# Kernel optimization log

Hardware: AMD Instinct MI355X
Metric: run time of the kernel (lower is better)

## Reference

```python
import jax, jax.numpy as jnp
import numpy as np

N_NODES = 20000
N_EDGES = 320000


def _gcn_conv(x, src, dst, dinv, W, b, n):
    # PyG GCNConv: h = x W; out[dst] += deg_src^-1/2 * deg_dst^-1/2 * h[src]; out += b
    h = x @ W                                  # [N, H]
    norm = dinv[src] * dinv[dst]               # [E+N]
    msg = h[src] * norm[:, None]               # [E+N, H]
    out = jax.ops.segment_sum(msg, dst, num_segments=n)
    return out + b


def setup_inputs() -> dict:
    key = jax.random.key(0)
    ks = jax.random.split(key, 11)
    d, c = 256, 3
    sc = 1.0 / np.sqrt(d)
    return {
        "x": jax.random.normal(ks[0], (N_NODES, d), dtype=jnp.float32),
        "edge_index": jax.random.randint(ks[1], (2, N_EDGES), 0, N_NODES, dtype=jnp.int64),
        "W_embed": jax.random.normal(ks[2], (d, d), dtype=jnp.float32) * sc,
        "b_embed": jax.random.normal(ks[3], (d,), dtype=jnp.float32) * 0.01,
        "W1": jax.random.normal(ks[4], (d, d), dtype=jnp.float32) * sc,
        "b1": jax.random.normal(ks[5], (d,), dtype=jnp.float32) * 0.01,
        "W2": jax.random.normal(ks[6], (d, d), dtype=jnp.float32) * sc,
        "b2": jax.random.normal(ks[7], (d,), dtype=jnp.float32) * 0.01,
        "W_cls": jax.random.normal(ks[8], (d, c), dtype=jnp.float32) * sc,
        "b_cls": jax.random.normal(ks[9], (c,), dtype=jnp.float32) * 0.01,
    }


def reference(x, edge_index, W_embed, b_embed, W1, b1, W2, b2, W_cls, b_cls):
    n = x.shape[0]
    # add self-loops once (GCNConv default add_self_loops=True)
    loops = jnp.arange(n, dtype=edge_index.dtype)
    src = jnp.concatenate([edge_index[0], loops])
    dst = jnp.concatenate([edge_index[1], loops])
    # symmetric normalization: degree computed on destination nodes
    deg = jnp.zeros((n,), dtype=x.dtype).at[dst].add(1.0)
    dinv = jax.lax.rsqrt(deg)  # deg >= 1 due to self loops

    h = jax.nn.relu(x @ W_embed + b_embed)
    h = _gcn_conv(h, src, dst, dinv, W1, b1, n)
    h = _gcn_conv(h, src, dst, dinv, W2, b2, n)
    logits = h @ W_cls + b_cls
    return logits
```

## Files before the change

kernel.cpp:

```cpp
#include <hip/hip_runtime.h>
#include <stdint.h>


typedef __attribute__((ext_vector_type(8))) __bf16 bf16x8;
typedef __attribute__((ext_vector_type(4))) float f32x4;

static __device__ __forceinline__ unsigned short f32_to_bf16(float f) {
  uint32_t u = __float_as_uint(f);
  u += 0x7fffu + ((u >> 16) & 1u);
  return (unsigned short)(u >> 16);
}
static __device__ __forceinline__ float bf16_to_f32(unsigned short h) {
  return __uint_as_float(((uint32_t)h) << 16);
}
static __device__ __forceinline__ int frag_addr(int m, int k) {
  return (((m >> 4) * 8 + (k >> 5)) << 9) + (((m & 15) + 16 * ((k >> 3) & 3)) << 3) + (k & 7);
}

__global__ void zero_ints(int* __restrict__ p, int n) {
  int i = blockIdx.x * blockDim.x + threadIdx.x;
  if (i < n) p[i] = 0;
}

__global__ void detect_i64(const unsigned int* __restrict__ ei, int nwords,
                           int* __restrict__ flag) {
  __shared__ int any;
  if (threadIdx.x == 0) any = 0;
  __syncthreads();
  for (int i = 1 + 2 * (int)threadIdx.x; i < nwords; i += 2 * blockDim.x)
    if (ei[i] != 0u) any = 1;
  __syncthreads();
  if (threadIdx.x == 0) *flag = (any == 0) ? 1 : 0;
}

__global__ void count_deg(const int* __restrict__ ei, int E,
                          const int* __restrict__ flag, int* __restrict__ cnt) {
  int e = blockIdx.x * blockDim.x + threadIdx.x;
  int is64 = *flag;
  if (e < E) {
    int d = is64 ? ei[2 * (E + e)] : ei[E + e];
    atomicAdd(&cnt[d], 1);
  }
}

__global__ __launch_bounds__(256) void scan_partials(
    const int* __restrict__ cnt, int* __restrict__ partials, int n) {
  __shared__ int sdata[256];
  int i = blockIdx.x * 256 + threadIdx.x;
  sdata[threadIdx.x] = (i < n) ? cnt[i] : 0;
  __syncthreads();
  for (int off = 128; off > 0; off >>= 1) {
    if (threadIdx.x < off) sdata[threadIdx.x] += sdata[threadIdx.x + off];
    __syncthreads();
  }
  if (threadIdx.x == 0) partials[blockIdx.x] = sdata[0];
}

__global__ __launch_bounds__(1024) void scan_offsets(int* __restrict__ partials,
                                                     int nb) {
  __shared__ int sdata[1024];
  int tid = threadIdx.x;
  sdata[tid] = (tid < nb) ? partials[tid] : 0;
  __syncthreads();
  for (int off = 1; off < 1024; off <<= 1) {
    int t = (tid >= off) ? sdata[tid - off] : 0;
    __syncthreads();
    sdata[tid] += t;
    __syncthreads();
  }
  if (tid < nb) partials[tid] = sdata[tid];
}

__global__ __launch_bounds__(256) void scan_finalize(
    const int* __restrict__ cnt, const int* __restrict__ partials_inc,
    int* __restrict__ row_ptr, float* __restrict__ dinv, int n) {
  __shared__ int sdata[256];
  int b = blockIdx.x;
  int i = b * 256 + threadIdx.x;
  int v = (i < n) ? cnt[i] : 0;
  sdata[threadIdx.x] = v;
  __syncthreads();
  for (int off = 1; off < 256; off <<= 1) {
    int t = (threadIdx.x >= off) ? sdata[threadIdx.x - off] : 0;
    __syncthreads();
    sdata[threadIdx.x] += t;
    __syncthreads();
  }
  int incl = sdata[threadIdx.x];
  int base = (b > 0) ? partials_inc[b - 1] : 0;
  if (i < n) {
    row_ptr[i] = base + incl - v;
    dinv[i] = 1.0f / sqrtf((float)(v + 1));
    if (i == n - 1) row_ptr[n] = base + incl;
  }
}

__global__ void fill_csr(const int* __restrict__ ei, int E,
                         const int* __restrict__ flag,
                         const int* __restrict__ row_ptr, int* __restrict__ cursor,
                         int* __restrict__ csr_src) {
  int e = blockIdx.x * blockDim.x + threadIdx.x;
  int is64 = *flag;
  if (e < E) {
    int s = is64 ? ei[2 * e] : ei[e];
    int d = is64 ? ei[2 * (E + e)] : ei[E + e];
    int pos = row_ptr[d] + atomicAdd(&cursor[d], 1);
    csr_src[pos] = s;
  }
}

__global__ void split_x_frag(const float4* __restrict__ in,
                             unsigned short* __restrict__ hi,
                             unsigned short* __restrict__ lo, int M) {
  int t = blockIdx.x * blockDim.x + threadIdx.x;
  if (t >= M * 32) return;
  int m = t >> 5, o = t & 31;
  float4 v0 = in[m * 64 + o * 2];
  float4 v1 = in[m * 64 + o * 2 + 1];
  float f[8] = {v0.x, v0.y, v0.z, v0.w, v1.x, v1.y, v1.z, v1.w};
  unsigned short hs[8], ls[8];
#pragma unroll
  for (int j = 0; j < 8; ++j) {
    unsigned short h = f32_to_bf16(f[j]);
    hs[j] = h;
    ls[j] = f32_to_bf16(f[j] - bf16_to_f32(h));
  }
  int addr = frag_addr(m, o * 8);
  *(ushort4*)(hi + addr) = make_ushort4(hs[0], hs[1], hs[2], hs[3]);
  *(ushort4*)(hi + addr + 4) = make_ushort4(hs[4], hs[5], hs[6], hs[7]);
  *(ushort4*)(lo + addr) = make_ushort4(ls[0], ls[1], ls[2], ls[3]);
  *(ushort4*)(lo + addr + 4) = make_ushort4(ls[4], ls[5], ls[6], ls[7]);
}

__global__ void pack_w_frag(const float* __restrict__ W,
                            unsigned short* __restrict__ hi,
                            unsigned short* __restrict__ lo) {
  int k = blockIdx.x, n = threadIdx.x;
  float v = W[k * 256 + n];
  unsigned short h = f32_to_bf16(v);
  int addr = frag_addr(n, k);
  hi[addr] = h;
  lo[addr] = f32_to_bf16(v - bf16_to_f32(h));
}

__global__ __launch_bounds__(256) void tail_matvec3(
    const float* __restrict__ A, const float* __restrict__ B3,
    float* __restrict__ O3) {
  int wid = threadIdx.x >> 6, lane = threadIdx.x & 63;
  int k = blockIdx.x * 4 + wid;
  float4 a = ((const float4*)(A + k * 256))[lane];
  int n0 = lane * 4;
  float s0 = a.x * B3[n0 * 3 + 0] + a.y * B3[n0 * 3 + 3] +
             a.z * B3[n0 * 3 + 6] + a.w * B3[n0 * 3 + 9];
  float s1 = a.x * B3[n0 * 3 + 1] + a.y * B3[n0 * 3 + 4] +
             a.z * B3[n0 * 3 + 7] + a.w * B3[n0 * 3 + 10];
  float s2 = a.x * B3[n0 * 3 + 2] + a.y * B3[n0 * 3 + 5] +
             a.z * B3[n0 * 3 + 8] + a.w * B3[n0 * 3 + 11];
#pragma unroll
  for (int off = 32; off > 0; off >>= 1) {
    s0 += __shfl_down(s0, off);
    s1 += __shfl_down(s1, off);
    s2 += __shfl_down(s2, off);
  }
  if (lane == 0) {
    O3[k * 3 + 0] = s0;
    O3[k * 3 + 1] = s1;
    O3[k * 3 + 2] = s2;
  }
}

__global__ __launch_bounds__(128) void tail_vec(
    const float* __restrict__ b1, const float* __restrict__ w2wc,
    const float* __restrict__ b2, const float* __restrict__ Wc,
    const float* __restrict__ bc, float* __restrict__ q,
    float* __restrict__ bvec) {
  int wid = threadIdx.x >> 6, lane = threadIdx.x & 63;
  const float* vin = (wid == 0) ? b1 : b2;
  const float* mat = (wid == 0) ? w2wc : Wc;
  float4 a = ((const float4*)vin)[lane];
  int n0 = lane * 4;
  float s0 = a.x * mat[n0 * 3 + 0] + a.y * mat[n0 * 3 + 3] +
             a.z * mat[n0 * 3 + 6] + a.w * mat[n0 * 3 + 9];
  float s1 = a.x * mat[n0 * 3 + 1] + a.y * mat[n0 * 3 + 4] +
             a.z * mat[n0 * 3 + 7] + a.w * mat[n0 * 3 + 10];
  float s2 = a.x * mat[n0 * 3 + 2] + a.y * mat[n0 * 3 + 5] +
             a.z * mat[n0 * 3 + 8] + a.w * mat[n0 * 3 + 11];
#pragma unroll
  for (int off = 32; off > 0; off >>= 1) {
    s0 += __shfl_down(s0, off);
    s1 += __shfl_down(s1, off);
    s2 += __shfl_down(s2, off);
  }
  if (lane == 0) {
    if (wid == 0) {
      q[0] = s0; q[1] = s1; q[2] = s2;
    } else {
      bvec[0] = s0 + bc[0]; bvec[1] = s1 + bc[1]; bvec[2] = s2 + bc[2];
    }
  }
}

__global__ __launch_bounds__(256) void gemm_u(
    const unsigned short* __restrict__ Ahi, const unsigned short* __restrict__ Alo,
    const unsigned short* __restrict__ Bhi, const unsigned short* __restrict__ Blo,
    int M, const float* __restrict__ bias, const float* __restrict__ P,
    float* __restrict__ u) {
  int wid = threadIdx.x >> 6, lane = threadIdx.x & 63;
  int wm = wid & 1, wn = wid >> 1;
  int Mtiles = (M + 15) >> 4;
  int mt_base = blockIdx.x * 4 + wm * 2;
  int nt_base = blockIdx.y * 8 + wn * 4;
  int la8 = lane * 8;

  int mt0 = mt_base < Mtiles ? mt_base : Mtiles - 1;
  int mt1 = mt_base + 1 < Mtiles ? mt_base + 1 : Mtiles - 1;
  const unsigned short* a0h = Ahi + mt0 * 4096 + la8;
  const unsigned short* a0l = Alo + mt0 * 4096 + la8;
  const unsigned short* a1h = Ahi + mt1 * 4096 + la8;
  const unsigned short* a1l = Alo + mt1 * 4096 + la8;
  const unsigned short* bh = Bhi + nt_base * 4096 + la8;
  const unsigned short* bl = Blo + nt_base * 4096 + la8;

  f32x4 acc[2][4] = {};
#pragma unroll
  for (int k0 = 0; k0 < 8; ++k0) {
    bf16x8 A0h = *(const bf16x8*)(a0h + k0 * 512);
    bf16x8 A0l = *(const bf16x8*)(a0l + k0 * 512);
    bf16x8 A1h = *(const bf16x8*)(a1h + k0 * 512);
    bf16x8 A1l = *(const bf16x8*)(a1l + k0 * 512);
#pragma unroll
    for (int ni = 0; ni < 4; ++ni) {
      bf16x8 Bh = *(const bf16x8*)(bh + ni * 4096 + k0 * 512);
      bf16x8 Bl = *(const bf16x8*)(bl + ni * 4096 + k0 * 512);
      acc[0][ni] = __builtin_amdgcn_mfma_f32_16x16x32_bf16(A0h, Bh, acc[0][ni], 0, 0, 0);
      acc[0][ni] = __builtin_amdgcn_mfma_f32_16x16x32_bf16(A0h, Bl, acc[0][ni], 0, 0, 0);
      acc[0][ni] = __builtin_amdgcn_mfma_f32_16x16x32_bf16(A0l, Bh, acc[0][ni], 0, 0, 0);
      acc[1][ni] = __builtin_amdgcn_mfma_f32_16x16x32_bf16(A1h, Bh, acc[1][ni], 0, 0, 0);
      acc[1][ni] = __builtin_amdgcn_mfma_f32_16x16x32_bf16(A1h, Bl, acc[1][ni], 0, 0, 0);
      acc[1][ni] = __builtin_amdgcn_mfma_f32_16x16x32_bf16(A1l, Bh, acc[1][ni], 0, 0, 0);
    }
  }

  int r = lane & 15, g = lane >> 4;
  float rp[8][3];
#pragma unroll
  for (int t = 0; t < 8; ++t) { rp[t][0] = 0.f; rp[t][1] = 0.f; rp[t][2] = 0.f; }
#pragma unroll
  for (int mi = 0; mi < 2; ++mi) {
#pragma unroll
    for (int ii = 0; ii < 4; ++ii) {
      int ri = mi * 4 + ii;
#pragma unroll
      for (int ni = 0; ni < 4; ++ni) {
        int col = (nt_base + ni) * 16 + r;
        float v = fmaxf(acc[mi][ni][ii] + bias[col], 0.0f);
        rp[ri][0] += v * P[col * 3 + 0];
        rp[ri][1] += v * P[col * 3 + 1];
        rp[ri][2] += v * P[col * 3 + 2];
      }
    }
  }
#pragma unroll
  for (int t = 0; t < 8; ++t) {
#pragma unroll
    for (int c = 0; c < 3; ++c) {
      float v = rp[t][c];
      v += __shfl_down(v, 8, 16);
      v += __shfl_down(v, 4, 16);
      v += __shfl_down(v, 2, 16);
      v += __shfl_down(v, 1, 16);
      rp[t][c] = v;
    }
  }
  if (r == 0) {
#pragma unroll
    for (int mi = 0; mi < 2; ++mi) {
#pragma unroll
      for (int ii = 0; ii < 4; ++ii) {
        int row = (mt_base + mi) * 16 + g * 4 + ii;
        if (row < M) {
          int ri = mi * 4 + ii;
          atomicAdd(&u[row * 3 + 0], rp[ri][0]);
          atomicAdd(&u[row * 3 + 1], rp[ri][1]);
          atomicAdd(&u[row * 3 + 2], rp[ri][2]);
        }
      }
    }
  }
}

__global__ void build_t4a(const float* __restrict__ u, const float* __restrict__ dinv,
                          float4* __restrict__ t4a, int n) {
  int i = blockIdx.x * blockDim.x + threadIdx.x;
  if (i >= n) return;
  float d = dinv[i];
  t4a[i] = make_float4(d * u[i * 3 + 0], d * u[i * 3 + 1], d * u[i * 3 + 2], d);
}

__global__ void conv_skinnyA(const float4* __restrict__ t4a,
                             const int* __restrict__ row_ptr,
                             const int* __restrict__ csr_src,
                             const float* __restrict__ dinv,
                             float4* __restrict__ t4b, int n) {
  int i = blockIdx.x * blockDim.x + threadIdx.x;
  if (i >= n) return;
  int e = row_ptr[i], e1 = row_ptr[i + 1];
  float a0 = 0.f, a1 = 0.f, a2 = 0.f, a3 = 0.f;
  float b0 = 0.f, b1 = 0.f, b2 = 0.f, b3 = 0.f;
  for (; e + 1 < e1; e += 2) {
    float4 v0 = t4a[csr_src[e]];
    float4 v1 = t4a[csr_src[e + 1]];
    a0 += v0.x; a1 += v0.y; a2 += v0.z; a3 += v0.w;
    b0 += v1.x; b1 += v1.y; b2 += v1.z; b3 += v1.w;
  }
  if (e < e1) {
    float4 v0 = t4a[csr_src[e]];
    a0 += v0.x; a1 += v0.y; a2 += v0.z; a3 += v0.w;
  }
  float4 self = t4a[i];
  float d = dinv[i];
  float d2 = d * d;
  t4b[i] = make_float4(d2 * (a0 + b0 + self.x), d2 * (a1 + b1 + self.y),
                       d2 * (a2 + b2 + self.z), d * (a3 + b3 + self.w));
}

__global__ void conv_skinnyB(const float4* __restrict__ t4b,
                             const int* __restrict__ row_ptr,
                             const int* __restrict__ csr_src,
                             const float* __restrict__ dinv,
                             const float* __restrict__ q,
                             const float* __restrict__ bvec,
                             float* __restrict__ out, int n) {
  int i = blockIdx.x * blockDim.x + threadIdx.x;
  if (i >= n) return;
  int e = row_ptr[i], e1 = row_ptr[i + 1];
  float a0 = 0.f, a1 = 0.f, a2 = 0.f;
  float b0 = 0.f, b1 = 0.f, b2 = 0.f;
  for (; e + 1 < e1; e += 2) {
    float4 v0 = t4b[csr_src[e]];
    float4 v1 = t4b[csr_src[e + 1]];
    a0 += v0.x; a1 += v0.y; a2 += v0.z;
    b0 += v1.x; b1 += v1.y; b2 += v1.z;
  }
  if (e < e1) {
    float4 v0 = t4b[csr_src[e]];
    a0 += v0.x; a1 += v0.y; a2 += v0.z;
  }
  float4 self = t4b[i];
  float d = dinv[i];
  float r = self.w;
  out[i * 3 + 0] = d * (a0 + b0 + self.x) + q[0] * r + bvec[0];
  out[i * 3 + 1] = d * (a1 + b1 + self.y) + q[1] * r + bvec[1];
  out[i * 3 + 2] = d * (a2 + b2 + self.z) + q[2] * r + bvec[2];
}

extern "C" void kernel_launch(void* const* d_in, const int* in_sizes, int n_in,
                              void* d_out, int out_size, void* d_ws, size_t ws_size,
                              hipStream_t stream) {
  const float* x = (const float*)d_in[0];
  const int* ei = (const int*)d_in[1];
  const float* W_embed = (const float*)d_in[2];
  const float* b_embed = (const float*)d_in[3];
  const float* W1 = (const float*)d_in[4];
  const float* b1 = (const float*)d_in[5];
  const float* W2 = (const float*)d_in[6];
  const float* b2 = (const float*)d_in[7];
  const float* Wcls = (const float*)d_in[8];
  const float* bcls = (const float*)d_in[9];
  const int N = in_sizes[0] / 256;
  const int E = in_sizes[1] / 2;

  char* ws = (char*)d_ws;
  size_t off = 0;
  auto alloc = [&](size_t bytes) {
    void* p = ws + off;
    off = (off + bytes + 255) & ~(size_t)255;
    return p;
  };
  int* cnt = (int*)alloc((size_t)N * 4);
  int* cursor = (int*)alloc((size_t)N * 4);
  int* row_ptr = (int*)alloc((size_t)(N + 1) * 4);
  float* dinv = (float*)alloc((size_t)N * 4);
  int* csr_src = (int*)alloc((size_t)E * 4);
  int* flag = (int*)alloc(256);
  int* partials = (int*)alloc(4096);
  unsigned short* WemFhi = (unsigned short*)alloc(256 * 256 * 2);
  unsigned short* WemFlo = (unsigned short*)alloc(256 * 256 * 2);
  float* w2wc = (float*)alloc(256 * 3 * 4);
  float* P = (float*)alloc(256 * 3 * 4);
  float* q = (float*)alloc(256);
  float* bvec = (float*)alloc(256);
  float* u = (float*)alloc((size_t)N * 3 * 4);
  float4* t4a = (float4*)alloc((size_t)N * 16);
  float4* t4b = (float4*)alloc((size_t)N * 16);
  size_t big = (size_t)N * 256;
  unsigned short* P1hi = (unsigned short*)alloc(big * 4);
  unsigned short* P1lo = P1hi + big;

  int nb = (N + 255) / 256;
  int nz = (int)(((char*)row_ptr - (char*)cnt) / 4);
  zero_ints<<<(nz + 255) / 256, 256, 0, stream>>>(cnt, nz);
  zero_ints<<<(N * 3 + 255) / 256, 256, 0, stream>>>((int*)u, N * 3);
  detect_i64<<<1, 256, 0, stream>>>((const unsigned int*)ei, 4096, flag);
  count_deg<<<(E + 255) / 256, 256, 0, stream>>>(ei, E, flag, cnt);
  scan_partials<<<nb, 256, 0, stream>>>(cnt, partials, N);
  scan_offsets<<<1, 1024, 0, stream>>>(partials, nb);
  scan_finalize<<<nb, 256, 0, stream>>>(cnt, partials, row_ptr, dinv, N);
  fill_csr<<<(E + 255) / 256, 256, 0, stream>>>(ei, E, flag, row_ptr, cursor, csr_src);

  split_x_frag<<<(N * 32 + 255) / 256, 256, 0, stream>>>((const float4*)x, P1hi, P1lo, N);
  pack_w_frag<<<256, 256, 0, stream>>>(W_embed, WemFhi, WemFlo);
  tail_matvec3<<<64, 256, 0, stream>>>(W2, Wcls, w2wc);
  tail_matvec3<<<64, 256, 0, stream>>>(W1, w2wc, P);
  tail_vec<<<1, 128, 0, stream>>>(b1, w2wc, b2, Wcls, bcls, q, bvec);

  dim3 gg((N + 63) / 64, 2);
  gemm_u<<<gg, 256, 0, stream>>>(P1hi, P1lo, WemFhi, WemFlo, N, b_embed, P, u);
  build_t4a<<<(N + 255) / 256, 256, 0, stream>>>(u, dinv, t4a, N);
  conv_skinnyA<<<(N + 255) / 256, 256, 0, stream>>>(t4a, row_ptr, csr_src, dinv,
                                                    t4b, N);
  conv_skinnyB<<<(N + 255) / 256, 256, 0, stream>>>(t4b, row_ptr, csr_src, dinv,
                                                    q, bvec, (float*)d_out, N);
}
```

Measured before the change: 186.9 us.

## Fuse build_t4a into gemm_u and drop atomics via full-N tiles per block

Each GEMM block now covers all 256 output columns (two waves along N with 8 tiles each) instead of splitting N across grid.y. The per-row projections are reduced in LDS and the block writes t4a directly with the dinv scaling. This removes the atomicAdd accumulation into u, the zeroing kernel and the separate build_t4a kernel. In exchange, each wave holds twice as many accumulators, which raises register pressure, and the grid has half as many blocks.

```diff
diff --git a/kernel.cpp b/kernel.cpp
--- a/kernel.cpp
+++ b/kernel.cpp
@@ -204,12 +204,12 @@
     const unsigned short* __restrict__ Ahi, const unsigned short* __restrict__ Alo,
     const unsigned short* __restrict__ Bhi, const unsigned short* __restrict__ Blo,
     int M, const float* __restrict__ bias, const float* __restrict__ P,
-    float* __restrict__ u) {
+    const float* __restrict__ dinv, float4* __restrict__ t4a) {
+  __shared__ float lds_u[2][64][3];
   int wid = threadIdx.x >> 6, lane = threadIdx.x & 63;
   int wm = wid & 1, wn = wid >> 1;
   int Mtiles = (M + 15) >> 4;
   int mt_base = blockIdx.x * 4 + wm * 2;
-  int nt_base = blockIdx.y * 8 + wn * 4;
   int la8 = lane * 8;
 
   int mt0 = mt_base < Mtiles ? mt_base : Mtiles - 1;
@@ -218,10 +218,10 @@
   const unsigned short* a0l = Alo + mt0 * 4096 + la8;
   const unsigned short* a1h = Ahi + mt1 * 4096 + la8;
   const unsigned short* a1l = Alo + mt1 * 4096 + la8;
-  const unsigned short* bh = Bhi + nt_base * 4096 + la8;
-  const unsigned short* bl = Blo + nt_base * 4096 + la8;
-
-  f32x4 acc[2][4] = {};
+  const unsigned short* bh = Bhi + wn * 8 * 4096 + la8;
+  const unsigned short* bl = Blo + wn * 8 * 4096 + la8;
+
+  f32x4 acc[2][8] = {};
 #pragma unroll
   for (int k0 = 0; k0 < 8; ++k0) {
     bf16x8 A0h = *(const bf16x8*)(a0h + k0 * 512);
@@ -229,7 +229,7 @@
     bf16x8 A1h = *(const bf16x8*)(a1h + k0 * 512);
     bf16x8 A1l = *(const bf16x8*)(a1l + k0 * 512);
 #pragma unroll
-    for (int ni = 0; ni < 4; ++ni) {
+    for (int ni = 0; ni < 8; ++ni) {
       bf16x8 Bh = *(const bf16x8*)(bh + ni * 4096 + k0 * 512);
       bf16x8 Bl = *(const bf16x8*)(bl + ni * 4096 + k0 * 512);
       acc[0][ni] = __builtin_amdgcn_mfma_f32_16x16x32_bf16(A0h, Bh, acc[0][ni], 0, 0, 0);
@@ -251,8 +251,8 @@
     for (int ii = 0; ii < 4; ++ii) {
       int ri = mi * 4 + ii;
 #pragma unroll
-      for (int ni = 0; ni < 4; ++ni) {
-        int col = (nt_base + ni) * 16 + r;
+      for (int ni = 0; ni < 8; ++ni) {
+        int col = (wn * 8 + ni) * 16 + r;
         float v = fmaxf(acc[mi][ni][ii] + bias[col], 0.0f);
         rp[ri][0] += v * P[col * 3 + 0];
         rp[ri][1] += v * P[col * 3 + 1];
@@ -277,24 +277,26 @@
     for (int mi = 0; mi < 2; ++mi) {
 #pragma unroll
       for (int ii = 0; ii < 4; ++ii) {
-        int row = (mt_base + mi) * 16 + g * 4 + ii;
-        if (row < M) {
-          int ri = mi * 4 + ii;
-          atomicAdd(&u[row * 3 + 0], rp[ri][0]);
-          atomicAdd(&u[row * 3 + 1], rp[ri][1]);
-          atomicAdd(&u[row * 3 + 2], rp[ri][2]);
-        }
+        int lrow = wm * 32 + mi * 16 + g * 4 + ii;
+        int ri = mi * 4 + ii;
+        lds_u[wn][lrow][0] = rp[ri][0];
+        lds_u[wn][lrow][1] = rp[ri][1];
+        lds_u[wn][lrow][2] = rp[ri][2];
       }
     }
   }
-}
-
-__global__ void build_t4a(const float* __restrict__ u, const float* __restrict__ dinv,
-                          float4* __restrict__ t4a, int n) {
-  int i = blockIdx.x * blockDim.x + threadIdx.x;
-  if (i >= n) return;
-  float d = dinv[i];
-  t4a[i] = make_float4(d * u[i * 3 + 0], d * u[i * 3 + 1], d * u[i * 3 + 2], d);
+  __syncthreads();
+  int t = threadIdx.x;
+  if (t < 64) {
+    int grow = blockIdx.x * 64 + t;
+    if (grow < M) {
+      float d = dinv[grow];
+      float u0 = lds_u[0][t][0] + lds_u[1][t][0];
+      float u1 = lds_u[0][t][1] + lds_u[1][t][1];
+      float u2 = lds_u[0][t][2] + lds_u[1][t][2];
+      t4a[grow] = make_float4(d * u0, d * u1, d * u2, d);
+    }
+  }
 }
 
 __global__ void conv_skinnyA(const float4* __restrict__ t4a,
@@ -390,7 +392,6 @@
   float* P = (float*)alloc(256 * 3 * 4);
   float* q = (float*)alloc(256);
   float* bvec = (float*)alloc(256);
-  float* u = (float*)alloc((size_t)N * 3 * 4);
   float4* t4a = (float4*)alloc((size_t)N * 16);
   float4* t4b = (float4*)alloc((size_t)N * 16);
   size_t big = (size_t)N * 256;
@@ -400,7 +401,6 @@
   int nb = (N + 255) / 256;
   int nz = (int)(((char*)row_ptr - (char*)cnt) / 4);
   zero_ints<<<(nz + 255) / 256, 256, 0, stream>>>(cnt, nz);
-  zero_ints<<<(N * 3 + 255) / 256, 256, 0, stream>>>((int*)u, N * 3);
   detect_i64<<<1, 256, 0, stream>>>((const unsigned int*)ei, 4096, flag);
   count_deg<<<(E + 255) / 256, 256, 0, stream>>>(ei, E, flag, cnt);
   scan_partials<<<nb, 256, 0, stream>>>(cnt, partials, N);
@@ -414,9 +414,8 @@
   tail_matvec3<<<64, 256, 0, stream>>>(W1, w2wc, P);
   tail_vec<<<1, 128, 0, stream>>>(b1, w2wc, b2, Wcls, bcls, q, bvec);
 
-  dim3 gg((N + 63) / 64, 2);
-  gemm_u<<<gg, 256, 0, stream>>>(P1hi, P1lo, WemFhi, WemFlo, N, b_embed, P, u);
-  build_t4a<<<(N + 255) / 256, 256, 0, stream>>>(u, dinv, t4a, N);
+  gemm_u<<<(N + 63) / 64, 256, 0, stream>>>(P1hi, P1lo, WemFhi, WemFlo, N,
+                                            b_embed, P, dinv, t4a);
   conv_skinnyA<<<(N + 255) / 256, 256, 0, stream>>>(t4a, row_ptr, csr_src, dinv,
                                                     t4b, N);
   conv_skinnyB<<<(N + 255) / 256, 256, 0, stream>>>(t4b, row_ptr, csr_src, dinv,
```

Result: slower. 192.7 us (+3.1%).
